# Optimization experiments

Hardware: AMD Instinct MI355X
Metric: run time of the kernel (lower is better)

The kernel has to match this reference:

```python
import jax, jax.numpy as jnp
import numpy as np
from jax.ops import segment_sum

N_NODES = 10000
N_EDGES = 320000


def leaky_relu(x):
    return jnp.where(x >= 0, x, 0.01 * x)


def gcn_layer(edge_h, src, dst, W, b):
    # (1) node h = mean of incoming edge features
    deg = segment_sum(jnp.ones((edge_h.shape[0],), edge_h.dtype), dst, num_segments=N_NODES)
    deg = jnp.maximum(deg, 1.0)
    h = segment_sum(edge_h, dst, num_segments=N_NODES) / deg[:, None]
    # (2) update_all: node h = sum over in-edges of src node h
    h2 = segment_sum(h[src], dst, num_segments=N_NODES)
    # (3) edge h = mean of endpoint node features
    eh = 0.5 * (h2[src] + h2[dst])
    # (4) linear on edge features
    return eh @ W.T + b


def setup_inputs() -> dict:
    key = jax.random.key(0)
    ks = jax.random.split(key, 20)
    d_in, d_h, d_out = 128, 256, 64
    inp = {
        'inputs1': jax.random.normal(ks[0], (N_EDGES, d_in), jnp.float32),
        'src1': jax.random.randint(ks[1], (N_EDGES,), 0, N_NODES, jnp.int32),
        'dst1': jax.random.randint(ks[2], (N_EDGES,), 0, N_NODES, jnp.int32),
        'inputs2': jax.random.normal(ks[3], (N_EDGES, d_in), jnp.float32),
        'src2': jax.random.randint(ks[4], (N_EDGES,), 0, N_NODES, jnp.int32),
        'dst2': jax.random.randint(ks[5], (N_EDGES,), 0, N_NODES, jnp.int32),
        'W11': jax.random.normal(ks[6], (d_h, d_in), jnp.float32) * 0.05,
        'b11': jax.random.normal(ks[7], (d_h,), jnp.float32) * 0.05,
        'W12': jax.random.normal(ks[8], (d_h, d_h), jnp.float32) * 0.05,
        'b12': jax.random.normal(ks[9], (d_h,), jnp.float32) * 0.05,
        'W21': jax.random.normal(ks[10], (d_h, d_in), jnp.float32) * 0.05,
        'b21': jax.random.normal(ks[11], (d_h,), jnp.float32) * 0.05,
        'W22': jax.random.normal(ks[12], (d_h, d_h), jnp.float32) * 0.05,
        'b22': jax.random.normal(ks[13], (d_h,), jnp.float32) * 0.05,
        'W3': jax.random.normal(ks[14], (d_out, 2 * d_h), jnp.float32) * 0.05,
        'b3': jax.random.normal(ks[15], (d_out,), jnp.float32) * 0.05,
    }
    return inp


def reference(inputs1, src1, dst1, inputs2, src2, dst2,
              W11, b11, W12, b12, W21, b21, W22, b22, W3, b3):
    h1 = leaky_relu(gcn_layer(inputs1, src1, dst1, W11, b11))
    h1 = leaky_relu(gcn_layer(h1, src1, dst1, W12, b12))
    h1 = jnp.mean(h1, axis=0)
    h2 = leaky_relu(gcn_layer(inputs2, src2, dst2, W21, b21))
    h2 = leaky_relu(gcn_layer(h2, src2, dst2, W22, b22))
    h2 = jnp.mean(h2, axis=0)
    out = jnp.concatenate((h1, h2), axis=0)
    return out @ W3.T + b3
```

## Files before the change

### kernel.cpp

```cpp
#include <hip/hip_runtime.h>
#include <cstddef>

#define NN 10000
#define NB 2500

typedef unsigned int u32;
typedef unsigned short u16;
typedef __attribute__((ext_vector_type(8))) short short8;
typedef __attribute__((ext_vector_type(4))) float f32x4;

__device__ __forceinline__ float bf_lo(u32 v) { union { u32 i; float f; } c; c.i = v << 16; return c.f; }
__device__ __forceinline__ float bf_hi(u32 v) { union { u32 i; float f; } c; c.i = v & 0xFFFF0000u; return c.f; }
__device__ __forceinline__ u32 rne_bits(float f) {
  union { float f; u32 i; } c; c.f = f;
  return c.i + 0x7FFFu + ((c.i >> 16) & 1u);
}
__device__ __forceinline__ u32 pack2(float a, float b) {
  return (rne_bits(a) >> 16) | (rne_bits(b) & 0xFFFF0000u);
}
__device__ __forceinline__ float lrmax(float x) { return fmaxf(x, 0.01f * x); }

__global__ __launch_bounds__(256) void wconv_kernel(
    const float* __restrict__ a, const float* __restrict__ b,
    const float* __restrict__ c, const float* __restrict__ d,
    u16* __restrict__ oa, u16* __restrict__ ob,
    u16* __restrict__ oc, u16* __restrict__ od,
    int* __restrict__ degbase ) {
  int i = blockIdx.x * 256 + threadIdx.x;
  if (i < 32768) oa[i] = (u16)(rne_bits(a[i]) >> 16);
  else if (i < 98304) ob[i - 32768] = (u16)(rne_bits(b[i - 32768]) >> 16);
  else if (i < 131072) oc[i - 98304] = (u16)(rne_bits(c[i - 98304]) >> 16);
  else if (i < 196608) od[i - 131072] = (u16)(rne_bits(d[i - 131072]) >> 16);
  if (i < 4 * NN) degbase[i] = 0;
}

__global__ __launch_bounds__(256) void count_b_kernel(const int* __restrict__ dstA,
                                                      const int* __restrict__ dstB,
                                                      int* __restrict__ degbase, int E) {
  const int g = blockIdx.y;
  const int* dst = g ? dstB : dstA;
  int* degi = degbase + (size_t)g * 2 * NN;
  int e = blockIdx.x * 256 + threadIdx.x;
  if (e < E) atomicAdd(&degi[dst[e]], 1);
}

__global__ __launch_bounds__(1024) void scan_b_kernel(const int* __restrict__ degbase,
                                                      int* __restrict__ offbase,
                                                      float* __restrict__ rdegbase, int n) {
  const int g = blockIdx.x;
  const int* degi = degbase + (size_t)g * 2 * NN;
  int* off = offbase + (size_t)g * NN;
  float* rdeg = rdegbase + (size_t)g * NN;
  __shared__ int wsum[16];
  __shared__ int wpre[16];
  __shared__ int carry_s;
  const int tid = threadIdx.x;
  const int lane = tid & 63, w = tid >> 6;
  if (tid == 0) carry_s = 0;
  __syncthreads();
  for (int base = 0; base < n; base += 1024) {
    int i = base + tid;
    int x = (i < n) ? degi[i] : 0;
    int v = x;
#pragma unroll
    for (int d = 1; d < 64; d <<= 1) {
      int t = __shfl_up(v, d);
      if (lane >= d) v += t;
    }
    if (lane == 63) wsum[w] = v;
    __syncthreads();
    if (tid == 0) {
      int s = carry_s;
#pragma unroll
      for (int j = 0; j < 16; ++j) { int t = wsum[j]; wpre[j] = s; s += t; }
      carry_s = s;
    }
    __syncthreads();
    if (i < n) {
      off[i] = wpre[w] + (v - x);
      rdeg[i] = 1.0f / fmaxf((float)x, 1.0f);
    }
    __syncthreads();
  }
}

__global__ __launch_bounds__(256) void fill_b_kernel(const int* __restrict__ srcA,
                                                     const int* __restrict__ dstA,
                                                     const int* __restrict__ srcB,
                                                     const int* __restrict__ dstB,
                                                     const int* __restrict__ offbase,
                                                     int* __restrict__ degbase,
                                                     int* __restrict__ eid_sb,
                                                     int* __restrict__ esrc_sb, int E) {
  const int g = blockIdx.y;
  const int* src = g ? srcB : srcA;
  const int* dst = g ? dstB : dstA;
  const int* off = offbase + (size_t)g * NN;
  int* cursor = degbase + (size_t)g * 2 * NN + NN;
  int* eid_s = eid_sb + (size_t)g * E;
  int* esrc_s = esrc_sb + (size_t)g * E;
  int e = blockIdx.x * 256 + threadIdx.x;
  if (e < E) {
    int d = dst[e];
    int p = off[d] + atomicAdd(&cursor[d], 1);
    eid_s[p] = e;
    esrc_s[p] = src[e];
  }
}

__global__ __launch_bounds__(256) void gatherA_b_kernel(
    const float* __restrict__ featA, const float* __restrict__ featB,
    const int* __restrict__ gidxb, const int* __restrict__ offbase,
    const int* __restrict__ degbase, const float* __restrict__ rdegbase,
    u32* __restrict__ outbfb , int E) {
  const int g = blockIdx.y;
  const float* feat = g ? featB : featA;
  const int* gidx = gidxb + (size_t)g * E;
  const int* off = offbase + (size_t)g * NN;
  const int* degi = degbase + (size_t)g * 2 * NN;
  const float* rdeg = rdegbase + (size_t)g * NN;
  u32* outbf = outbfb + (size_t)g * NN * 64;
  const int n = (blockIdx.x << 2) + (threadIdx.x >> 6);
  const int lane = threadIdx.x & 63;
  const int hl = lane & 31, h = lane >> 5;
  const int o = off[n], d = degi[n];
  const int fo = hl << 2;
  float4 acc = make_float4(0.f, 0.f, 0.f, 0.f);
  for (int c0 = 0; c0 < d; c0 += 64) {
    const int m = min(64, d - c0);
    const int gg = (lane < m) ? gidx[o + c0 + lane] : 0;
    const int pairs = m >> 1;
    int i = 0;
    for (; i + 4 <= pairs; i += 4) {
      const int e0 = 2 * i + h;
      const int s0 = __shfl(gg, e0), s1 = __shfl(gg, e0 + 2);
      const int s2 = __shfl(gg, e0 + 4), s3 = __shfl(gg, e0 + 6);
      const float4 v0 = *(const float4*)&feat[(s0 << 7) + fo];
      const float4 v1 = *(const float4*)&feat[(s1 << 7) + fo];
      const float4 v2 = *(const float4*)&feat[(s2 << 7) + fo];
      const float4 v3 = *(const float4*)&feat[(s3 << 7) + fo];
      acc.x += (v0.x + v1.x) + (v2.x + v3.x);
      acc.y += (v0.y + v1.y) + (v2.y + v3.y);
      acc.z += (v0.z + v1.z) + (v2.z + v3.z);
      acc.w += (v0.w + v1.w) + (v2.w + v3.w);
    }
    for (; i < pairs; ++i) {
      const int s0 = __shfl(gg, 2 * i + h);
      const float4 v0 = *(const float4*)&feat[(s0 << 7) + fo];
      acc.x += v0.x; acc.y += v0.y; acc.z += v0.z; acc.w += v0.w;
    }
    if (m & 1) {
      const int s0 = __shfl(gg, m - 1);
      const float wgt = (h == 0) ? 1.f : 0.f;
      const float4 v0 = *(const float4*)&feat[(s0 << 7) + fo];
      acc.x = fmaf(v0.x, wgt, acc.x);
      acc.y = fmaf(v0.y, wgt, acc.y);
      acc.z = fmaf(v0.z, wgt, acc.z);
      acc.w = fmaf(v0.w, wgt, acc.w);
    }
  }
  acc.x += __shfl(acc.x, lane ^ 32);
  acc.y += __shfl(acc.y, lane ^ 32);
  acc.z += __shfl(acc.z, lane ^ 32);
  acc.w += __shfl(acc.w, lane ^ 32);
  if (h == 0) {
    const float sc = rdeg[n];
    uint2 r;
    r.x = pack2(acc.x * sc, acc.y * sc);
    r.y = pack2(acc.z * sc, acc.w * sc);
    *(uint2*)&outbf[(size_t)n * 64 + (hl << 1)] = r;
  }
}

#define QREDUCE8(aL, aH)                                                   \
  aL.x += __shfl(aL.x, lane ^ 16); aL.y += __shfl(aL.y, lane ^ 16);        \
  aL.z += __shfl(aL.z, lane ^ 16); aL.w += __shfl(aL.w, lane ^ 16);        \
  aH.x += __shfl(aH.x, lane ^ 16); aH.y += __shfl(aH.y, lane ^ 16);        \
  aH.z += __shfl(aH.z, lane ^ 16); aH.w += __shfl(aH.w, lane ^ 16);        \
  aL.x += __shfl(aL.x, lane ^ 32); aL.y += __shfl(aL.y, lane ^ 32);        \
  aL.z += __shfl(aL.z, lane ^ 32); aL.w += __shfl(aL.w, lane ^ 32);        \
  aH.x += __shfl(aH.x, lane ^ 32); aH.y += __shfl(aH.y, lane ^ 32);        \
  aH.z += __shfl(aH.z, lane ^ 32); aH.w += __shfl(aH.w, lane ^ 32);

__global__ __launch_bounds__(256) void gatherB_b_kernel(
    const u32* __restrict__ featb , const int* __restrict__ gidxb,
    const int* __restrict__ offbase, const int* __restrict__ degbase,
    u32* __restrict__ outbfb, int E) {
  const int bid = blockIdx.x;
  const int r = bid & 7, t = bid >> 3;
  const int g = r >> 2;
  const int nb = t * 4 + (r & 3);
  const u32* feat = featb + (size_t)g * NN * 64;
  const int* gidx = gidxb + (size_t)g * E;
  const int* off = offbase + (size_t)g * NN;
  const int* degi = degbase + (size_t)g * 2 * NN;
  u32* outbf = outbfb + (size_t)g * NN * 64;
  const int n = (nb << 2) + (threadIdx.x >> 6);
  const int lane = threadIdx.x & 63;
  const int q = lane >> 4, ql = lane & 15;
  const int o = off[n], d = degi[n];
  const int fo = ql << 2;
  float4 aL = make_float4(0.f, 0.f, 0.f, 0.f), aH = make_float4(0.f, 0.f, 0.f, 0.f);
  for (int c0 = 0; c0 < d; c0 += 64) {
    const int m = min(64, d - c0);
    const int gg = (lane < m) ? gidx[o + c0 + lane] : 0;
    const int full = m >> 2;
    int i = 0;
    for (; i + 2 <= full; i += 2) {
      const int e0 = 4 * i + q;
      const int s0 = __shfl(gg, e0), s1 = __shfl(gg, e0 + 4);
      const uint4 v0 = *(const uint4*)&feat[(s0 << 6) + fo];
      const uint4 v1 = *(const uint4*)&feat[(s1 << 6) + fo];
      aL.x += bf_lo(v0.x) + bf_lo(v1.x); aL.y += bf_hi(v0.x) + bf_hi(v1.x);
      aL.z += bf_lo(v0.y) + bf_lo(v1.y); aL.w += bf_hi(v0.y) + bf_hi(v1.y);
      aH.x += bf_lo(v0.z) + bf_lo(v1.z); aH.y += bf_hi(v0.z) + bf_hi(v1.z);
      aH.z += bf_lo(v0.w) + bf_lo(v1.w); aH.w += bf_hi(v0.w) + bf_hi(v1.w);
    }
    if (i < full) {
      const int s0 = __shfl(gg, 4 * i + q);
      const uint4 v0 = *(const uint4*)&feat[(s0 << 6) + fo];
      aL.x += bf_lo(v0.x); aL.y += bf_hi(v0.x);
      aL.z += bf_lo(v0.y); aL.w += bf_hi(v0.y);
      aH.x += bf_lo(v0.z); aH.y += bf_hi(v0.z);
      aH.z += bf_lo(v0.w); aH.w += bf_hi(v0.w);
    }
    if (m & 3) {
      const int e = (m & ~3) + q;
      const int s0 = __shfl(gg, e < m ? e : (m - 1));
      const float wgt = (e < m) ? 1.f : 0.f;
      const uint4 v0 = *(const uint4*)&feat[(s0 << 6) + fo];
      aL.x = fmaf(bf_lo(v0.x), wgt, aL.x); aL.y = fmaf(bf_hi(v0.x), wgt, aL.y);
      aL.z = fmaf(bf_lo(v0.y), wgt, aL.z); aL.w = fmaf(bf_hi(v0.y), wgt, aL.w);
      aH.x = fmaf(bf_lo(v0.z), wgt, aH.x); aH.y = fmaf(bf_hi(v0.z), wgt, aH.y);
      aH.z = fmaf(bf_lo(v0.w), wgt, aH.z); aH.w = fmaf(bf_hi(v0.w), wgt, aH.w);
    }
  }
  QREDUCE8(aL, aH)
  if (lane < 16) {
    uint4 outv;
    outv.x = pack2(aL.x, aL.y);
    outv.y = pack2(aL.z, aL.w);
    outv.z = pack2(aH.x, aH.y);
    outv.w = pack2(aH.z, aH.w);
    *(uint4*)&outbf[(n << 6) + fo] = outv;
  }
}

__device__ __forceinline__ void acc_lr8(float4& aL, float4& aH, uint4 v,
                                        const float4& wL, const float4& wH) {
  float u;
  u = fmaf(bf_lo(v.x), 0.5f, wL.x); aL.x += lrmax(u);
  u = fmaf(bf_hi(v.x), 0.5f, wL.y); aL.y += lrmax(u);
  u = fmaf(bf_lo(v.y), 0.5f, wL.z); aL.z += lrmax(u);
  u = fmaf(bf_hi(v.y), 0.5f, wL.w); aL.w += lrmax(u);
  u = fmaf(bf_lo(v.z), 0.5f, wH.x); aH.x += lrmax(u);
  u = fmaf(bf_hi(v.z), 0.5f, wH.y); aH.y += lrmax(u);
  u = fmaf(bf_lo(v.w), 0.5f, wH.z); aH.z += lrmax(u);
  u = fmaf(bf_hi(v.w), 0.5f, wH.w); aH.w += lrmax(u);
}
__device__ __forceinline__ void acc_lr8w(float4& aL, float4& aH, uint4 v,
                                         const float4& wL, const float4& wH, float wgt) {
  float u;
  u = fmaf(bf_lo(v.x), 0.5f, wL.x); aL.x = fmaf(lrmax(u), wgt, aL.x);
  u = fmaf(bf_hi(v.x), 0.5f, wL.y); aL.y = fmaf(lrmax(u), wgt, aL.y);
  u = fmaf(bf_lo(v.y), 0.5f, wL.z); aL.z = fmaf(lrmax(u), wgt, aL.z);
  u = fmaf(bf_hi(v.y), 0.5f, wL.w); aL.w = fmaf(lrmax(u), wgt, aL.w);
  u = fmaf(bf_lo(v.z), 0.5f, wH.x); aH.x = fmaf(lrmax(u), wgt, aH.x);
  u = fmaf(bf_hi(v.z), 0.5f, wH.y); aH.y = fmaf(lrmax(u), wgt, aH.y);
  u = fmaf(bf_lo(v.w), 0.5f, wH.z); aH.z = fmaf(lrmax(u), wgt, aH.z);
  u = fmaf(bf_hi(v.w), 0.5f, wH.w); aH.w = fmaf(lrmax(u), wgt, aH.w);
}

__global__ __launch_bounds__(256) void passC_b_kernel(
    const u32* __restrict__ Zb_, const int* __restrict__ esrcb,
    const int* __restrict__ offbase, const int* __restrict__ degbase,
    const float* __restrict__ rdegbase,
    const float* __restrict__ biasA, const float* __restrict__ biasB,
    u32* __restrict__ hBb, int E) {
  const int bid = blockIdx.x;
  const int r = bid & 7, t = bid >> 3;
  const int g = r >> 2, fh = (r >> 1) & 1;
  const int nb = t * 2 + (r & 1);
  const u32* Z = Zb_ + (size_t)g * NN * 128;
  const int* esrc = esrcb + (size_t)g * E;
  const int* off = offbase + (size_t)g * NN;
  const int* degi = degbase + (size_t)g * 2 * NN;
  const float* rdeg = rdegbase + (size_t)g * NN;
  const float* bias = g ? biasB : biasA;
  u32* hB = hBb + (size_t)g * NN * 128;
  const int n = (nb << 2) + (threadIdx.x >> 6);
  const int lane = threadIdx.x & 63;
  const int q = lane >> 4, ql = lane & 15;
  const int o = off[n], d = degi[n];
  const int fo = (fh << 6) + (ql << 2);
  const uint4 znv = *(const uint4*)&Z[(n << 7) + fo];
  const float4 bL = *(const float4*)&bias[(fh << 7) + (ql << 3)];
  const float4 bH = *(const float4*)&bias[(fh << 7) + (ql << 3) + 4];
  float4 wL, wH;
  wL.x = fmaf(bf_lo(znv.x), 0.5f, bL.x); wL.y = fmaf(bf_hi(znv.x), 0.5f, bL.y);
  wL.z = fmaf(bf_lo(znv.y), 0.5f, bL.z); wL.w = fmaf(bf_hi(znv.y), 0.5f, bL.w);
  wH.x = fmaf(bf_lo(znv.z), 0.5f, bH.x); wH.y = fmaf(bf_hi(znv.z), 0.5f, bH.y);
  wH.z = fmaf(bf_lo(znv.w), 0.5f, bH.z); wH.w = fmaf(bf_hi(znv.w), 0.5f, bH.w);
  float4 aL = make_float4(0.f, 0.f, 0.f, 0.f), aH = make_float4(0.f, 0.f, 0.f, 0.f);
  for (int c0 = 0; c0 < d; c0 += 64) {
    const int m = min(64, d - c0);
    const int gg = (lane < m) ? esrc[o + c0 + lane] : 0;
    const int full = m >> 2;
    int i = 0;
    for (; i + 2 <= full; i += 2) {
      const int e0 = 4 * i + q;
      const int s0 = __shfl(gg, e0), s1 = __shfl(gg, e0 + 4);
      const uint4 z0 = *(const uint4*)&Z[(s0 << 7) + fo];
      const uint4 z1 = *(const uint4*)&Z[(s1 << 7) + fo];
      acc_lr8(aL, aH, z0, wL, wH);
      acc_lr8(aL, aH, z1, wL, wH);
    }
    if (i < full) {
      const int s0 = __shfl(gg, 4 * i + q);
      const uint4 z0 = *(const uint4*)&Z[(s0 << 7) + fo];
      acc_lr8(aL, aH, z0, wL, wH);
    }
    if (m & 3) {
      const int e = (m & ~3) + q;
      const int s0 = __shfl(gg, e < m ? e : (m - 1));
      const float wgt = (e < m) ? 1.f : 0.f;
      const uint4 z0 = *(const uint4*)&Z[(s0 << 7) + fo];
      acc_lr8w(aL, aH, z0, wL, wH, wgt);
    }
  }
  QREDUCE8(aL, aH)
  if (lane < 16) {
    const float rr = rdeg[n];
    uint4 outv;
    outv.x = pack2(aL.x * rr, aL.y * rr);
    outv.y = pack2(aL.z * rr, aL.w * rr);
    outv.z = pack2(aH.x * rr, aH.y * rr);
    outv.w = pack2(aH.z * rr, aH.w * rr);
    *(uint4*)&hB[(n << 7) + fo] = outv;
  }
}

__global__ __launch_bounds__(256) void gatherC_b_kernel(
    const u32* __restrict__ featb , const int* __restrict__ gidxb,
    const int* __restrict__ offbase, const int* __restrict__ degbase,
    u32* __restrict__ outbfb, int E) {
  const int bid = blockIdx.x;
  const int r = bid & 7, t = bid >> 3;
  const int g = r >> 2, fh = (r >> 1) & 1;
  const int nb = t * 2 + (r & 1);
  const u32* feat = featb + (size_t)g * NN * 128;
  const int* gidx = gidxb + (size_t)g * E;
  const int* off = offbase + (size_t)g * NN;
  const int* degi = degbase + (size_t)g * 2 * NN;
  u32* outbf = outbfb + (size_t)g * NN * 128;
  const int n = (nb << 2) + (threadIdx.x >> 6);
  const int lane = threadIdx.x & 63;
  const int q = lane >> 4, ql = lane & 15;
  const int o = off[n], d = degi[n];
  const int fo = (fh << 6) + (ql << 2);
  float4 aL = make_float4(0.f, 0.f, 0.f, 0.f), aH = make_float4(0.f, 0.f, 0.f, 0.f);
  for (int c0 = 0; c0 < d; c0 += 64) {
    const int m = min(64, d - c0);
    const int gg = (lane < m) ? gidx[o + c0 + lane] : 0;
    const int full = m >> 2;
    int i = 0;
    for (; i + 2 <= full; i += 2) {
      const int e0 = 4 * i + q;
      const int s0 = __shfl(gg, e0), s1 = __shfl(gg, e0 + 4);
      const uint4 z0 = *(const uint4*)&feat[(s0 << 7) + fo];
      const uint4 z1 = *(const uint4*)&feat[(s1 << 7) + fo];
      aL.x += bf_lo(z0.x) + bf_lo(z1.x); aL.y += bf_hi(z0.x) + bf_hi(z1.x);
      aL.z += bf_lo(z0.y) + bf_lo(z1.y); aL.w += bf_hi(z0.y) + bf_hi(z1.y);
      aH.x += bf_lo(z0.z) + bf_lo(z1.z); aH.y += bf_hi(z0.z) + bf_hi(z1.z);
      aH.z += bf_lo(z0.w) + bf_lo(z1.w); aH.w += bf_hi(z0.w) + bf_hi(z1.w);
    }
    if (i < full) {
      const int s0 = __shfl(gg, 4 * i + q);
      const uint4 z0 = *(const uint4*)&feat[(s0 << 7) + fo];
      aL.x += bf_lo(z0.x); aL.y += bf_hi(z0.x);
      aL.z += bf_lo(z0.y); aL.w += bf_hi(z0.y);
      aH.x += bf_lo(z0.z); aH.y += bf_hi(z0.z);
      aH.z += bf_lo(z0.w); aH.w += bf_hi(z0.w);
    }
    if (m & 3) {
      const int e = (m & ~3) + q;
      const int s0 = __shfl(gg, e < m ? e : (m - 1));
      const float wgt = (e < m) ? 1.f : 0.f;
      const uint4 z0 = *(const uint4*)&feat[(s0 << 7) + fo];
      aL.x = fmaf(bf_lo(z0.x), wgt, aL.x); aL.y = fmaf(bf_hi(z0.x), wgt, aL.y);
      aL.z = fmaf(bf_lo(z0.y), wgt, aL.z); aL.w = fmaf(bf_hi(z0.y), wgt, aL.w);
      aH.x = fmaf(bf_lo(z0.z), wgt, aH.x); aH.y = fmaf(bf_hi(z0.z), wgt, aH.y);
      aH.z = fmaf(bf_lo(z0.w), wgt, aH.z); aH.w = fmaf(bf_hi(z0.w), wgt, aH.w);
    }
  }
  QREDUCE8(aL, aH)
  if (lane < 16) {
    uint4 outv;
    outv.x = pack2(aL.x, aL.y);
    outv.y = pack2(aL.z, aL.w);
    outv.z = pack2(aH.x, aH.y);
    outv.w = pack2(aH.z, aH.w);
    *(uint4*)&outbf[(n << 7) + fo] = outv;
  }
}

__global__ __launch_bounds__(256) void passE_b_kernel(
    const u32* __restrict__ Z2b, const int* __restrict__ esrcb,
    const int* __restrict__ offbase, const int* __restrict__ degbase,
    const float* __restrict__ biasA, const float* __restrict__ biasB,
    float* __restrict__ partialsb , int nNodes, int E) {
  const int bid = blockIdx.x;
  const int r = bid & 7, t = bid >> 3;
  const int g = r >> 2, fh = (r >> 1) & 1;
  const int blk = t * 2 + (r & 1);
  const u32* Z2 = Z2b + (size_t)g * NN * 128;
  const int* esrc = esrcb + (size_t)g * E;
  const int* off = offbase + (size_t)g * NN;
  const int* degi = degbase + (size_t)g * 2 * NN;
  const float* bias = g ? biasB : biasA;
  float* partials = partialsb + (size_t)((g * 2 + fh) * 128 + blk) * 128;
  const int lane = threadIdx.x & 63, w = threadIdx.x >> 6;
  const int q = lane >> 4, ql = lane & 15;
  const int fo = (fh << 6) + (ql << 2);
  const float4 bL = *(const float4*)&bias[(fh << 7) + (ql << 3)];
  const float4 bH = *(const float4*)&bias[(fh << 7) + (ql << 3) + 4];
  float4 aL = make_float4(0.f, 0.f, 0.f, 0.f), aH = make_float4(0.f, 0.f, 0.f, 0.f);
  for (int n = blk * 4 + w; n < nNodes; n += 512) {
    const int o = off[n], d = degi[n];
    const uint4 znv = *(const uint4*)&Z2[(n << 7) + fo];
    float4 wL, wH;
    wL.x = fmaf(bf_lo(znv.x), 0.5f, bL.x); wL.y = fmaf(bf_hi(znv.x), 0.5f, bL.y);
    wL.z = fmaf(bf_lo(znv.y), 0.5f, bL.z); wL.w = fmaf(bf_hi(znv.y), 0.5f, bL.w);
    wH.x = fmaf(bf_lo(znv.z), 0.5f, bH.x); wH.y = fmaf(bf_hi(znv.z), 0.5f, bH.y);
    wH.z = fmaf(bf_lo(znv.w), 0.5f, bH.z); wH.w = fmaf(bf_hi(znv.w), 0.5f, bH.w);
    for (int c0 = 0; c0 < d; c0 += 64) {
      const int m = min(64, d - c0);
      const int gg = (lane < m) ? esrc[o + c0 + lane] : 0;
      const int full = m >> 2;
      int i = 0;
      for (; i + 2 <= full; i += 2) {
        const int e0 = 4 * i + q;
        const int s0 = __shfl(gg, e0), s1 = __shfl(gg, e0 + 4);
        const uint4 z0 = *(const uint4*)&Z2[(s0 << 7) + fo];
        const uint4 z1 = *(const uint4*)&Z2[(s1 << 7) + fo];
        acc_lr8(aL, aH, z0, wL, wH);
        acc_lr8(aL, aH, z1, wL, wH);
      }
      if (i < full) {
        const int s0 = __shfl(gg, 4 * i + q);
        const uint4 z0 = *(const uint4*)&Z2[(s0 << 7) + fo];
        acc_lr8(aL, aH, z0, wL, wH);
      }
      if (m & 3) {
        const int e = (m & ~3) + q;
        const int s0 = __shfl(gg, e < m ? e : (m - 1));
        const float wgt = (e < m) ? 1.f : 0.f;
        const uint4 z0 = *(const uint4*)&Z2[(s0 << 7) + fo];
        acc_lr8w(aL, aH, z0, wL, wH, wgt);
      }
    }
  }
  QREDUCE8(aL, aH)
  __shared__ float red[4][128];
  if (lane < 16) {
    *(float4*)&red[w][ql << 3] = aL;
    *(float4*)&red[w][(ql << 3) + 4] = aH;
  }
  __syncthreads();
  const int tid = threadIdx.x;
  if (tid < 128) partials[tid] = red[0][tid] + red[1][tid] + red[2][tid] + red[3][tid];
}

__global__ __launch_bounds__(1024) void final_fused_kernel(
    const float* __restrict__ partialsb ,
    const float* __restrict__ W3, const float* __restrict__ b3,
    float* __restrict__ out, float invE) {
  __shared__ float smacc[512];
  __shared__ float tmp2[2][512];
  __shared__ float red[16][64];
  const int tid = threadIdx.x;
  {
    const int half = tid >> 9;
    const int q = tid & 511;
    const float* basep = partialsb + (size_t)(q >> 7) * 128 * 128 + (q & 127);
    float s = 0.f;
    for (int b = half * 64; b < half * 64 + 64; ++b) s += basep[(size_t)b * 128];
    tmp2[half][q] = s;
  }
  __syncthreads();
  if (tid < 512) smacc[tid] = tmp2[0][tid] + tmp2[1][tid];
  __syncthreads();
  const int j = tid & 63, part = tid >> 6;
  float acc = 0.f;
  for (int kk = 0; kk < 32; ++kk) {
    const int k = part * 32 + kk;
    acc += smacc[k] * W3[(size_t)j * 512 + k];
  }
  red[part][j] = acc;
  __syncthreads();
  if (part == 0) {
    float s = 0.f;
#pragma unroll
    for (int p = 0; p < 16; ++p) s += red[p][j];
    out[j] = b3[j] + s * invE;
  }
}

template <int K>
__global__ __launch_bounds__(256) void gemm_mfma_b_kernel(const u16* __restrict__ Ab,
                                                          const u16* __restrict__ WA,
                                                          const u16* __restrict__ WB,
                                                          u16* __restrict__ Cb, int N) {
  const int g = blockIdx.z;
  const u16* A = Ab + (size_t)g * NN * K;
  const u16* Wb = g ? WB : WA;
  u16* C = Cb + (size_t)g * NN * 256;
  const int lane = threadIdx.x & 63;
  const int w = threadIdx.x >> 6;
  const int wm = w >> 1, wn = w & 1;
  const int bn = blockIdx.x * 64 + wm * 32;
  const int bo = blockIdx.y * 64 + wn * 32;
  const int r0 = lane & 15;
  const int kq = lane >> 4;
  const int ra0 = min(bn + r0, N - 1);
  const int ra1 = min(bn + 16 + r0, N - 1);
  const u16* a0p = &A[(size_t)ra0 * K + kq * 8];
  const u16* a1p = &A[(size_t)ra1 * K + kq * 8];
  const u16* b0p = &Wb[(size_t)(bo + r0) * K + kq * 8];
  const u16* b1p = &Wb[(size_t)(bo + 16 + r0) * K + kq * 8];
  f32x4 acc00 = {0.f, 0.f, 0.f, 0.f}, acc01 = {0.f, 0.f, 0.f, 0.f};
  f32x4 acc10 = {0.f, 0.f, 0.f, 0.f}, acc11 = {0.f, 0.f, 0.f, 0.f};
#pragma unroll
  for (int k0 = 0; k0 < K; k0 += 32) {
    const short8 a0 = *(const short8*)(a0p + k0);
    const short8 a1 = *(const short8*)(a1p + k0);
    const short8 b0 = *(const short8*)(b0p + k0);
    const short8 b1 = *(const short8*)(b1p + k0);
    acc00 = __builtin_amdgcn_mfma_f32_16x16x32_bf16(a0, b0, acc00, 0, 0, 0);
    acc01 = __builtin_amdgcn_mfma_f32_16x16x32_bf16(a0, b1, acc01, 0, 0, 0);
    acc10 = __builtin_amdgcn_mfma_f32_16x16x32_bf16(a1, b0, acc10, 0, 0, 0);
    acc11 = __builtin_amdgcn_mfma_f32_16x16x32_bf16(a1, b1, acc11, 0, 0, 0);
  }
#pragma unroll
  for (int r = 0; r < 4; ++r) {
    const int n0 = bn + 4 * kq + r;
    if (n0 < N) {
      C[(size_t)n0 * 256 + bo + r0] = (u16)(rne_bits(acc00[r]) >> 16);
      C[(size_t)n0 * 256 + bo + 16 + r0] = (u16)(rne_bits(acc01[r]) >> 16);
    }
    const int n1 = bn + 16 + 4 * kq + r;
    if (n1 < N) {
      C[(size_t)n1 * 256 + bo + r0] = (u16)(rne_bits(acc10[r]) >> 16);
      C[(size_t)n1 * 256 + bo + 16 + r0] = (u16)(rne_bits(acc11[r]) >> 16);
    }
  }
}

extern "C" void kernel_launch(void* const* d_in, const int* in_sizes, int n_in,
                              void* d_out, int out_size, void* d_ws, size_t ws_size,
                              hipStream_t stream) {
  const float* in1 = (const float*)d_in[0];
  const int* src1 = (const int*)d_in[1];
  const int* dst1 = (const int*)d_in[2];
  const float* in2 = (const float*)d_in[3];
  const int* src2 = (const int*)d_in[4];
  const int* dst2 = (const int*)d_in[5];
  const float* W11 = (const float*)d_in[6];
  const float* b11 = (const float*)d_in[7];
  const float* W12 = (const float*)d_in[8];
  const float* b12 = (const float*)d_in[9];
  const float* W21 = (const float*)d_in[10];
  const float* b21 = (const float*)d_in[11];
  const float* W22 = (const float*)d_in[12];
  const float* b22 = (const float*)d_in[13];
  const float* W3 = (const float*)d_in[14];
  const float* b3 = (const float*)d_in[15];
  const int E = in_sizes[1];
  const int N = NN;

  char* base = (char*)d_ws;
  size_t pos = 0;
  auto carve = [&](size_t bytes) -> char* {
    char* p = base + pos;
    pos = (pos + bytes + 511) & ~(size_t)511;
    return p;
  };
  int* degbase = (int*)carve((size_t)2 * 2 * N * sizeof(int));
  int* offb = (int*)carve((size_t)2 * N * sizeof(int));
  float* rdegb = (float*)carve((size_t)2 * N * sizeof(float));
  int* eid_sb = (int*)carve((size_t)2 * E * sizeof(int));
  int* esrc_sb = (int*)carve((size_t)2 * E * sizeof(int));
  u32* Hb = (u32*)carve((size_t)2 * N * 64 * sizeof(u32));
  u32* H2b = (u32*)carve((size_t)2 * N * 64 * sizeof(u32));
  u32* Zb = (u32*)carve((size_t)2 * N * 128 * sizeof(u32));
  u32* HBb = (u32*)carve((size_t)2 * N * 128 * sizeof(u32));
  u32* H2Bb = (u32*)carve((size_t)2 * N * 128 * sizeof(u32));
  u16* Wa1 = (u16*)carve((size_t)32768 * sizeof(u16));
  u16* Wb1 = (u16*)carve((size_t)65536 * sizeof(u16));
  u16* Wa2 = (u16*)carve((size_t)32768 * sizeof(u16));
  u16* Wb2 = (u16*)carve((size_t)65536 * sizeof(u16));
  float* partialsb = (float*)carve((size_t)2 * 2 * 128 * 128 * sizeof(float));
  (void)ws_size; (void)n_in; (void)out_size;

  const int EB = (E + 255) / 256;
  const dim3 g2(EB, 2);
  const dim3 n2(NB, 2);
  const dim3 gemm_grid((N + 63) / 64, 4, 2);

  wconv_kernel<<<768, 256, 0, stream>>>(W11, W12, W21, W22, Wa1, Wb1, Wa2, Wb2, degbase);

  count_b_kernel<<<g2, 256, 0, stream>>>(dst1, dst2, degbase, E);
  scan_b_kernel<<<2, 1024, 0, stream>>>(degbase, offb, rdegb, N);
  fill_b_kernel<<<g2, 256, 0, stream>>>(src1, dst1, src2, dst2, offb, degbase, eid_sb, esrc_sb, E);

  gatherA_b_kernel<<<n2, 256, 0, stream>>>(in1, in2, eid_sb, offb, degbase, rdegb, Hb, E);
  gatherB_b_kernel<<<2 * NB, 256, 0, stream>>>(Hb, esrc_sb, offb, degbase, H2b, E);
  gemm_mfma_b_kernel<128><<<gemm_grid, 256, 0, stream>>>((const u16*)H2b, Wa1, Wa2, (u16*)Zb, N);

  passC_b_kernel<<<4 * NB, 256, 0, stream>>>(Zb, esrc_sb, offb, degbase, rdegb, b11, b21, HBb, E);
  gatherC_b_kernel<<<4 * NB, 256, 0, stream>>>(HBb, esrc_sb, offb, degbase, H2Bb, E);
  gemm_mfma_b_kernel<256><<<gemm_grid, 256, 0, stream>>>((const u16*)H2Bb, Wb1, Wb2, (u16*)Zb, N);

  passE_b_kernel<<<512, 256, 0, stream>>>(Zb, esrc_sb, offb, degbase, b12, b22, partialsb, N, E);
  final_fused_kernel<<<1, 1024, 0, stream>>>(partialsb, W3, b3, (float*)d_out, 1.0f / (float)E);
}
```

Baseline: 329.7 us.

## Skew the two graph pipelines and co-schedule independent stages in shared kernels

The per-kernel bodies become device functions. Instead of batching both graphs into each stage kernel, graph 2's stages now run offset from graph 1's. Heterogeneous fused kernels dispatch on block index, so graph 2's gathers run in the same grid as graph 1's passC, gatherC and GEMM stages, and graph 2's first GEMM shares a grid with graph 1's final reduction. The goal is to fill small or tail-heavy grids (the GEMMs and the reduction pass) with independent work. In exchange the launch count grows and the later graph 2 stages run alone.

```diff
diff --git a/kernel.cpp b/kernel.cpp
--- a/kernel.cpp
+++ b/kernel.cpp
@@ -2,7 +2,6 @@
 #include <cstddef>
 
 #define NN 10000
-#define NB 2500
 
 typedef unsigned int u32;
 typedef unsigned short u16;
@@ -25,7 +24,7 @@
     const float* __restrict__ c, const float* __restrict__ d,
     u16* __restrict__ oa, u16* __restrict__ ob,
     u16* __restrict__ oc, u16* __restrict__ od,
-    int* __restrict__ degbase ) {
+    int* __restrict__ degbase) {
   int i = blockIdx.x * 256 + threadIdx.x;
   if (i < 32768) oa[i] = (u16)(rne_bits(a[i]) >> 16);
   else if (i < 98304) ob[i - 32768] = (u16)(rne_bits(b[i - 32768]) >> 16);
@@ -108,20 +107,12 @@
   }
 }
 
-__global__ __launch_bounds__(256) void gatherA_b_kernel(
-    const float* __restrict__ featA, const float* __restrict__ featB,
-    const int* __restrict__ gidxb, const int* __restrict__ offbase,
-    const int* __restrict__ degbase, const float* __restrict__ rdegbase,
-    u32* __restrict__ outbfb , int E) {
-  const int g = blockIdx.y;
-  const float* feat = g ? featB : featA;
-  const int* gidx = gidxb + (size_t)g * E;
-  const int* off = offbase + (size_t)g * NN;
-  const int* degi = degbase + (size_t)g * 2 * NN;
-  const float* rdeg = rdegbase + (size_t)g * NN;
-  u32* outbf = outbfb + (size_t)g * NN * 64;
-  const int n = (blockIdx.x << 2) + (threadIdx.x >> 6);
-  const int lane = threadIdx.x & 63;
+
+__device__ __forceinline__ void dev_A(int n, int tid, const float* __restrict__ feat,
+                                      const int* __restrict__ gidx, const int* __restrict__ off,
+                                      const int* __restrict__ degi, const float* __restrict__ rdeg,
+                                      u32* __restrict__ outbf) {
+  const int lane = tid & 63;
   const int hl = lane & 31, h = lane >> 5;
   const int o = off[n], d = degi[n];
   const int fo = hl << 2;
@@ -182,21 +173,10 @@
   aH.x += __shfl(aH.x, lane ^ 32); aH.y += __shfl(aH.y, lane ^ 32);        \
   aH.z += __shfl(aH.z, lane ^ 32); aH.w += __shfl(aH.w, lane ^ 32);
 
-__global__ __launch_bounds__(256) void gatherB_b_kernel(
-    const u32* __restrict__ featb , const int* __restrict__ gidxb,
-    const int* __restrict__ offbase, const int* __restrict__ degbase,
-    u32* __restrict__ outbfb, int E) {
-  const int bid = blockIdx.x;
-  const int r = bid & 7, t = bid >> 3;
-  const int g = r >> 2;
-  const int nb = t * 4 + (r & 3);
-  const u32* feat = featb + (size_t)g * NN * 64;
-  const int* gidx = gidxb + (size_t)g * E;
-  const int* off = offbase + (size_t)g * NN;
-  const int* degi = degbase + (size_t)g * 2 * NN;
-  u32* outbf = outbfb + (size_t)g * NN * 64;
-  const int n = (nb << 2) + (threadIdx.x >> 6);
-  const int lane = threadIdx.x & 63;
+__device__ __forceinline__ void dev_B(int n, int tid, const u32* __restrict__ feat,
+                                      const int* __restrict__ gidx, const int* __restrict__ off,
+                                      const int* __restrict__ degi, u32* __restrict__ outbf) {
+  const int lane = tid & 63;
   const int q = lane >> 4, ql = lane & 15;
   const int o = off[n], d = degi[n];
   const int fo = ql << 2;
@@ -271,25 +251,11 @@
   u = fmaf(bf_hi(v.w), 0.5f, wH.w); aH.w = fmaf(lrmax(u), wgt, aH.w);
 }
 
-__global__ __launch_bounds__(256) void passC_b_kernel(
-    const u32* __restrict__ Zb_, const int* __restrict__ esrcb,
-    const int* __restrict__ offbase, const int* __restrict__ degbase,
-    const float* __restrict__ rdegbase,
-    const float* __restrict__ biasA, const float* __restrict__ biasB,
-    u32* __restrict__ hBb, int E) {
-  const int bid = blockIdx.x;
-  const int r = bid & 7, t = bid >> 3;
-  const int g = r >> 2, fh = (r >> 1) & 1;
-  const int nb = t * 2 + (r & 1);
-  const u32* Z = Zb_ + (size_t)g * NN * 128;
-  const int* esrc = esrcb + (size_t)g * E;
-  const int* off = offbase + (size_t)g * NN;
-  const int* degi = degbase + (size_t)g * 2 * NN;
-  const float* rdeg = rdegbase + (size_t)g * NN;
-  const float* bias = g ? biasB : biasA;
-  u32* hB = hBb + (size_t)g * NN * 128;
-  const int n = (nb << 2) + (threadIdx.x >> 6);
-  const int lane = threadIdx.x & 63;
+__device__ __forceinline__ void dev_C(int n, int fh, int tid, const u32* __restrict__ Z,
+                                      const int* __restrict__ esrc, const int* __restrict__ off,
+                                      const int* __restrict__ degi, const float* __restrict__ rdeg,
+                                      const float* __restrict__ bias, u32* __restrict__ hB) {
+  const int lane = tid & 63;
   const int q = lane >> 4, ql = lane & 15;
   const int o = off[n], d = degi[n];
   const int fo = (fh << 6) + (ql << 2);
@@ -340,21 +306,10 @@
   }
 }
 
-__global__ __launch_bounds__(256) void gatherC_b_kernel(
-    const u32* __restrict__ featb , const int* __restrict__ gidxb,
-    const int* __restrict__ offbase, const int* __restrict__ degbase,
-    u32* __restrict__ outbfb, int E) {
-  const int bid = blockIdx.x;
-  const int r = bid & 7, t = bid >> 3;
-  const int g = r >> 2, fh = (r >> 1) & 1;
-  const int nb = t * 2 + (r & 1);
-  const u32* feat = featb + (size_t)g * NN * 128;
-  const int* gidx = gidxb + (size_t)g * E;
-  const int* off = offbase + (size_t)g * NN;
-  const int* degi = degbase + (size_t)g * 2 * NN;
-  u32* outbf = outbfb + (size_t)g * NN * 128;
-  const int n = (nb << 2) + (threadIdx.x >> 6);
-  const int lane = threadIdx.x & 63;
+__device__ __forceinline__ void dev_C2(int n, int fh, int tid, const u32* __restrict__ feat,
+                                       const int* __restrict__ gidx, const int* __restrict__ off,
+                                       const int* __restrict__ degi, u32* __restrict__ outbf) {
+  const int lane = tid & 63;
   const int q = lane >> 4, ql = lane & 15;
   const int o = off[n], d = degi[n];
   const int fo = (fh << 6) + (ql << 2);
@@ -404,28 +359,17 @@
   }
 }
 
-__global__ __launch_bounds__(256) void passE_b_kernel(
-    const u32* __restrict__ Z2b, const int* __restrict__ esrcb,
-    const int* __restrict__ offbase, const int* __restrict__ degbase,
-    const float* __restrict__ biasA, const float* __restrict__ biasB,
-    float* __restrict__ partialsb , int nNodes, int E) {
-  const int bid = blockIdx.x;
-  const int r = bid & 7, t = bid >> 3;
-  const int g = r >> 2, fh = (r >> 1) & 1;
-  const int blk = t * 2 + (r & 1);
-  const u32* Z2 = Z2b + (size_t)g * NN * 128;
-  const int* esrc = esrcb + (size_t)g * E;
-  const int* off = offbase + (size_t)g * NN;
-  const int* degi = degbase + (size_t)g * 2 * NN;
-  const float* bias = g ? biasB : biasA;
-  float* partials = partialsb + (size_t)((g * 2 + fh) * 128 + blk) * 128;
-  const int lane = threadIdx.x & 63, w = threadIdx.x >> 6;
+__device__ __forceinline__ void dev_E(int blk, int fh, int tid, const u32* __restrict__ Z2,
+                                      const int* __restrict__ esrc, const int* __restrict__ off,
+                                      const int* __restrict__ degi, const float* __restrict__ bias,
+                                      float* __restrict__ partials ) {
+  const int lane = tid & 63, w = tid >> 6;
   const int q = lane >> 4, ql = lane & 15;
   const int fo = (fh << 6) + (ql << 2);
   const float4 bL = *(const float4*)&bias[(fh << 7) + (ql << 3)];
   const float4 bH = *(const float4*)&bias[(fh << 7) + (ql << 3) + 4];
   float4 aL = make_float4(0.f, 0.f, 0.f, 0.f), aH = make_float4(0.f, 0.f, 0.f, 0.f);
-  for (int n = blk * 4 + w; n < nNodes; n += 512) {
+  for (int n = blk * 4 + w; n < NN; n += 512) {
     const int o = off[n], d = degi[n];
     const uint4 znv = *(const uint4*)&Z2[(n << 7) + fo];
     float4 wL, wH;
@@ -467,8 +411,168 @@
     *(float4*)&red[w][(ql << 3) + 4] = aH;
   }
   __syncthreads();
-  const int tid = threadIdx.x;
   if (tid < 128) partials[tid] = red[0][tid] + red[1][tid] + red[2][tid] + red[3][tid];
+}
+
+template <int K>
+__device__ __forceinline__ void dev_gemm(int bx, int by, int tid, const u16* __restrict__ A,
+                                         const u16* __restrict__ W, u16* __restrict__ C) {
+  const int lane = tid & 63;
+  const int w = tid >> 6;
+  const int wm = w >> 1, wn = w & 1;
+  const int bn = bx * 64 + wm * 32;
+  const int bo = by * 64 + wn * 32;
+  const int r0 = lane & 15;
+  const int kq = lane >> 4;
+  const int ra0 = min(bn + r0, NN - 1);
+  const int ra1 = min(bn + 16 + r0, NN - 1);
+  const u16* a0p = &A[(size_t)ra0 * K + kq * 8];
+  const u16* a1p = &A[(size_t)ra1 * K + kq * 8];
+  const u16* b0p = &W[(size_t)(bo + r0) * K + kq * 8];
+  const u16* b1p = &W[(size_t)(bo + 16 + r0) * K + kq * 8];
+  f32x4 acc00 = {0.f, 0.f, 0.f, 0.f}, acc01 = {0.f, 0.f, 0.f, 0.f};
+  f32x4 acc10 = {0.f, 0.f, 0.f, 0.f}, acc11 = {0.f, 0.f, 0.f, 0.f};
+#pragma unroll
+  for (int k0 = 0; k0 < K; k0 += 32) {
+    const short8 a0 = *(const short8*)(a0p + k0);
+    const short8 a1 = *(const short8*)(a1p + k0);
+    const short8 b0 = *(const short8*)(b0p + k0);
+    const short8 b1 = *(const short8*)(b1p + k0);
+    acc00 = __builtin_amdgcn_mfma_f32_16x16x32_bf16(a0, b0, acc00, 0, 0, 0);
+    acc01 = __builtin_amdgcn_mfma_f32_16x16x32_bf16(a0, b1, acc01, 0, 0, 0);
+    acc10 = __builtin_amdgcn_mfma_f32_16x16x32_bf16(a1, b0, acc10, 0, 0, 0);
+    acc11 = __builtin_amdgcn_mfma_f32_16x16x32_bf16(a1, b1, acc11, 0, 0, 0);
+  }
+#pragma unroll
+  for (int r = 0; r < 4; ++r) {
+    const int n0 = bn + 4 * kq + r;
+    if (n0 < NN) {
+      C[(size_t)n0 * 256 + bo + r0] = (u16)(rne_bits(acc00[r]) >> 16);
+      C[(size_t)n0 * 256 + bo + 16 + r0] = (u16)(rne_bits(acc01[r]) >> 16);
+    }
+    const int n1 = bn + 16 + 4 * kq + r;
+    if (n1 < NN) {
+      C[(size_t)n1 * 256 + bo + r0] = (u16)(rne_bits(acc10[r]) >> 16);
+      C[(size_t)n1 * 256 + bo + 16 + r0] = (u16)(rne_bits(acc11[r]) >> 16);
+    }
+  }
+}
+
+
+__global__ __launch_bounds__(256) void kA_kernel(const float* __restrict__ feat,
+                                                 const int* gidx, const int* off,
+                                                 const int* degi, const float* rdeg,
+                                                 u32* __restrict__ outbf) {
+  dev_A((blockIdx.x << 2) + (threadIdx.x >> 6), threadIdx.x, feat, gidx, off, degi, rdeg, outbf);
+}
+
+__global__ __launch_bounds__(256) void kF_B_A(const u32* featB_, const int* gidxB, const int* offB,
+                                              const int* degB, u32* outB,
+                                              const float* featA_, const int* gidxA, const int* offA,
+                                              const int* degA, const float* rdegA, u32* outA,
+                                              int aBase) {
+  const int bid = blockIdx.x;
+  if (bid < 625) {
+    dev_A(aBase + (bid << 2) + (threadIdx.x >> 6), threadIdx.x, featA_, gidxA, offA, degA, rdegA, outA);
+  } else {
+    dev_B(((bid - 625) << 2) + (threadIdx.x >> 6), threadIdx.x, featB_, gidxB, offB, degB, outB);
+  }
+}
+
+template <int K>
+__global__ __launch_bounds__(256) void kF_G_A(const u16* Ag, const u16* W, u16* Cg,
+                                              const float* featA_, const int* gidxA, const int* offA,
+                                              const int* degA, const float* rdegA, u32* outA,
+                                              int aBase) {
+  const int bid = blockIdx.x;
+  if (bid < 625) {
+    dev_A(aBase + (bid << 2) + (threadIdx.x >> 6), threadIdx.x, featA_, gidxA, offA, degA, rdegA, outA);
+  } else {
+    const int gb = bid - 625;
+    dev_gemm<K>(gb >> 2, gb & 3, threadIdx.x, Ag, W, Cg);
+  }
+}
+
+__global__ __launch_bounds__(256) void kF_C_A(const u32* Z, const int* esrc, const int* off,
+                                              const int* degi, const float* rdeg, const float* bias,
+                                              u32* hB,
+                                              const float* featA_, const int* gidxA, const int* offA,
+                                              const int* degA, const float* rdegA, u32* outA,
+                                              int aBase) {
+  const int bid = blockIdx.x;
+  if (bid < 625) {
+    dev_A(aBase + (bid << 2) + (threadIdx.x >> 6), threadIdx.x, featA_, gidxA, offA, degA, rdegA, outA);
+  } else {
+    const int cb = bid - 625;
+    const int fh = cb >= 2500;
+    dev_C(((fh ? cb - 2500 : cb) << 2) + (threadIdx.x >> 6), fh, threadIdx.x, Z, esrc, off, degi,
+          rdeg, bias, hB);
+  }
+}
+__global__ __launch_bounds__(256) void kF_C2_A(const u32* feat, const int* gidx, const int* off,
+                                               const int* degi, u32* outbf,
+                                               const float* featA_, const int* gidxA, const int* offA,
+                                               const int* degA, const float* rdegA, u32* outA,
+                                               int aBase) {
+  const int bid = blockIdx.x;
+  if (bid < 625) {
+    dev_A(aBase + (bid << 2) + (threadIdx.x >> 6), threadIdx.x, featA_, gidxA, offA, degA, rdegA, outA);
+  } else {
+    const int cb = bid - 625;
+    const int fh = cb >= 2500;
+    dev_C2(((fh ? cb - 2500 : cb) << 2) + (threadIdx.x >> 6), fh, threadIdx.x, feat, gidx, off,
+           degi, outbf);
+  }
+}
+
+__global__ __launch_bounds__(256) void kF_G2_B(const u16* Ag, const u16* W, u16* Cg,
+                                               const u32* featB_, const int* gidxB, const int* offB,
+                                               const int* degB, u32* outB) {
+  const int bid = blockIdx.x;
+  if (bid < 2500) {
+    dev_B((bid << 2) + (threadIdx.x >> 6), threadIdx.x, featB_, gidxB, offB, degB, outB);
+  } else {
+    const int gb = bid - 2500;
+    dev_gemm<256>(gb >> 2, gb & 3, threadIdx.x, Ag, W, Cg);
+  }
+}
+
+__global__ __launch_bounds__(256) void kF_E_G(const u32* Z2, const int* esrc, const int* off,
+                                              const int* degi, const float* bias, float* partials,
+                                              const u16* Ag, const u16* W, u16* Cg) {
+  const int bid = blockIdx.x;
+  if (bid < 628) {
+    dev_gemm<128>(bid >> 2, bid & 3, threadIdx.x, Ag, W, Cg);
+  } else {
+    const int eb = bid - 628;
+    const int fh = eb >> 7, blk = eb & 127;
+    dev_E(blk, fh, threadIdx.x, Z2, esrc, off, degi, bias, partials + (size_t)(fh * 128 + blk) * 128);
+  }
+}
+
+__global__ __launch_bounds__(256) void kC_kernel(const u32* Z, const int* esrc, const int* off,
+                                                 const int* degi, const float* rdeg,
+                                                 const float* bias, u32* hB) {
+  const int bid = blockIdx.x;
+  const int fh = bid >= 2500;
+  dev_C(((fh ? bid - 2500 : bid) << 2) + (threadIdx.x >> 6), fh, threadIdx.x, Z, esrc, off, degi,
+        rdeg, bias, hB);
+}
+__global__ __launch_bounds__(256) void kC2_kernel(const u32* feat, const int* gidx, const int* off,
+                                                  const int* degi, u32* outbf) {
+  const int bid = blockIdx.x;
+  const int fh = bid >= 2500;
+  dev_C2(((fh ? bid - 2500 : bid) << 2) + (threadIdx.x >> 6), fh, threadIdx.x, feat, gidx, off,
+         degi, outbf);
+}
+__global__ __launch_bounds__(256) void kG_kernel256(const u16* Ag, const u16* W, u16* Cg) {
+  dev_gemm<256>(blockIdx.x >> 2, blockIdx.x & 3, threadIdx.x, Ag, W, Cg);
+}
+__global__ __launch_bounds__(256) void kE_kernel(const u32* Z2, const int* esrc, const int* off,
+                                                 const int* degi, const float* bias,
+                                                 float* partials) {
+  const int fh = blockIdx.x >> 7, blk = blockIdx.x & 127;
+  dev_E(blk, fh, threadIdx.x, Z2, esrc, off, degi, bias, partials + (size_t)(fh * 128 + blk) * 128);
 }
 
 __global__ __launch_bounds__(1024) void final_fused_kernel(
@@ -503,56 +607,6 @@
 #pragma unroll
     for (int p = 0; p < 16; ++p) s += red[p][j];
     out[j] = b3[j] + s * invE;
-  }
-}
-
-template <int K>
-__global__ __launch_bounds__(256) void gemm_mfma_b_kernel(const u16* __restrict__ Ab,
-                                                          const u16* __restrict__ WA,
-                                                          const u16* __restrict__ WB,
-                                                          u16* __restrict__ Cb, int N) {
-  const int g = blockIdx.z;
-  const u16* A = Ab + (size_t)g * NN * K;
-  const u16* Wb = g ? WB : WA;
-  u16* C = Cb + (size_t)g * NN * 256;
-  const int lane = threadIdx.x & 63;
-  const int w = threadIdx.x >> 6;
-  const int wm = w >> 1, wn = w & 1;
-  const int bn = blockIdx.x * 64 + wm * 32;
-  const int bo = blockIdx.y * 64 + wn * 32;
-  const int r0 = lane & 15;
-  const int kq = lane >> 4;
-  const int ra0 = min(bn + r0, N - 1);
-  const int ra1 = min(bn + 16 + r0, N - 1);
-  const u16* a0p = &A[(size_t)ra0 * K + kq * 8];
-  const u16* a1p = &A[(size_t)ra1 * K + kq * 8];
-  const u16* b0p = &Wb[(size_t)(bo + r0) * K + kq * 8];
-  const u16* b1p = &Wb[(size_t)(bo + 16 + r0) * K + kq * 8];
-  f32x4 acc00 = {0.f, 0.f, 0.f, 0.f}, acc01 = {0.f, 0.f, 0.f, 0.f};
-  f32x4 acc10 = {0.f, 0.f, 0.f, 0.f}, acc11 = {0.f, 0.f, 0.f, 0.f};
-#pragma unroll
-  for (int k0 = 0; k0 < K; k0 += 32) {
-    const short8 a0 = *(const short8*)(a0p + k0);
-    const short8 a1 = *(const short8*)(a1p + k0);
-    const short8 b0 = *(const short8*)(b0p + k0);
-    const short8 b1 = *(const short8*)(b1p + k0);
-    acc00 = __builtin_amdgcn_mfma_f32_16x16x32_bf16(a0, b0, acc00, 0, 0, 0);
-    acc01 = __builtin_amdgcn_mfma_f32_16x16x32_bf16(a0, b1, acc01, 0, 0, 0);
-    acc10 = __builtin_amdgcn_mfma_f32_16x16x32_bf16(a1, b0, acc10, 0, 0, 0);
-    acc11 = __builtin_amdgcn_mfma_f32_16x16x32_bf16(a1, b1, acc11, 0, 0, 0);
-  }
-#pragma unroll
-  for (int r = 0; r < 4; ++r) {
-    const int n0 = bn + 4 * kq + r;
-    if (n0 < N) {
-      C[(size_t)n0 * 256 + bo + r0] = (u16)(rne_bits(acc00[r]) >> 16);
-      C[(size_t)n0 * 256 + bo + 16 + r0] = (u16)(rne_bits(acc01[r]) >> 16);
-    }
-    const int n1 = bn + 16 + 4 * kq + r;
-    if (n1 < N) {
-      C[(size_t)n1 * 256 + bo + r0] = (u16)(rne_bits(acc10[r]) >> 16);
-      C[(size_t)n1 * 256 + bo + 16 + r0] = (u16)(rne_bits(acc11[r]) >> 16);
-    }
   }
 }
 
@@ -602,25 +656,43 @@
   float* partialsb = (float*)carve((size_t)2 * 2 * 128 * 128 * sizeof(float));
   (void)ws_size; (void)n_in; (void)out_size;
 
+  const int* off0 = offb;            const int* off1 = offb + N;
+  const int* deg0 = degbase;         const int* deg1 = degbase + 2 * N;
+  const float* rdeg0 = rdegb;        const float* rdeg1 = rdegb + N;
+  const int* eid0 = eid_sb;          const int* eid1 = eid_sb + E;
+  const int* esrc0 = esrc_sb;        const int* esrc1 = esrc_sb + E;
+  u32* H0 = Hb;                      u32* H1 = Hb + (size_t)N * 64;
+  u32* H20 = H2b;                    u32* H21 = H2b + (size_t)N * 64;
+  u32* Z0 = Zb;                      u32* Z1 = Zb + (size_t)N * 128;
+  u32* HB0 = HBb;                    u32* HB1 = HBb + (size_t)N * 128;
+  u32* H2B0 = H2Bb;                  u32* H2B1 = H2Bb + (size_t)N * 128;
+  float* part0 = partialsb;          float* part1 = partialsb + 2 * 128 * 128;
+
   const int EB = (E + 255) / 256;
   const dim3 g2(EB, 2);
-  const dim3 n2(NB, 2);
-  const dim3 gemm_grid((N + 63) / 64, 4, 2);
 
   wconv_kernel<<<768, 256, 0, stream>>>(W11, W12, W21, W22, Wa1, Wb1, Wa2, Wb2, degbase);
-
   count_b_kernel<<<g2, 256, 0, stream>>>(dst1, dst2, degbase, E);
   scan_b_kernel<<<2, 1024, 0, stream>>>(degbase, offb, rdegb, N);
   fill_b_kernel<<<g2, 256, 0, stream>>>(src1, dst1, src2, dst2, offb, degbase, eid_sb, esrc_sb, E);
 
-  gatherA_b_kernel<<<n2, 256, 0, stream>>>(in1, in2, eid_sb, offb, degbase, rdegb, Hb, E);
-  gatherB_b_kernel<<<2 * NB, 256, 0, stream>>>(Hb, esrc_sb, offb, degbase, H2b, E);
-  gemm_mfma_b_kernel<128><<<gemm_grid, 256, 0, stream>>>((const u16*)H2b, Wa1, Wa2, (u16*)Zb, N);
-
-  passC_b_kernel<<<4 * NB, 256, 0, stream>>>(Zb, esrc_sb, offb, degbase, rdegb, b11, b21, HBb, E);
-  gatherC_b_kernel<<<4 * NB, 256, 0, stream>>>(HBb, esrc_sb, offb, degbase, H2Bb, E);
-  gemm_mfma_b_kernel<256><<<gemm_grid, 256, 0, stream>>>((const u16*)H2Bb, Wb1, Wb2, (u16*)Zb, N);
-
-  passE_b_kernel<<<512, 256, 0, stream>>>(Zb, esrc_sb, offb, degbase, b12, b22, partialsb, N, E);
+  kA_kernel<<<2500, 256, 0, stream>>>(in1, eid0, off0, deg0, rdeg0, H0);
+  kF_B_A<<<3125, 256, 0, stream>>>(H0, esrc0, off0, deg0, H20,
+                                   in2, eid1, off1, deg1, rdeg1, H1, 0);
+  kF_G_A<128><<<1253, 256, 0, stream>>>((const u16*)H20, Wa1, (u16*)Z0,
+                                        in2, eid1, off1, deg1, rdeg1, H1, 2500);
+  kF_C_A<<<5625, 256, 0, stream>>>(Z0, esrc0, off0, deg0, rdeg0, b11, HB0,
+                                   in2, eid1, off1, deg1, rdeg1, H1, 5000);
+  kF_C2_A<<<5625, 256, 0, stream>>>(HB0, esrc0, off0, deg0, H2B0,
+                                    in2, eid1, off1, deg1, rdeg1, H1, 7500);
+  kF_G2_B<<<3128, 256, 0, stream>>>((const u16*)H2B0, Wb1, (u16*)Z0,
+                                    H1, esrc1, off1, deg1, H21);
+  kF_E_G<<<884, 256, 0, stream>>>(Z0, esrc0, off0, deg0, b12, part0,
+                                  (const u16*)H21, Wa2, (u16*)Z1);
+  kC_kernel<<<5000, 256, 0, stream>>>(Z1, esrc1, off1, deg1, rdeg1, b21, HB1);
+  kC2_kernel<<<5000, 256, 0, stream>>>(HB1, esrc1, off1, deg1, H2B1);
+  kG_kernel256<<<628, 256, 0, stream>>>((const u16*)H2B1, Wb2, (u16*)Z1);
+  kE_kernel<<<256, 256, 0, stream>>>(Z1, esrc1, off1, deg1, b22, part1);
+
   final_fused_kernel<<<1, 1024, 0, stream>>>(partialsb, W3, b3, (float*)d_out, 1.0f / (float)E);
 }
```

Result: slower. 422.5 us (+28.1%).
